# Performance work log

Measured on AMD Instinct MI355X. Metric: run time of the kernel, lower is better.

The kernel has to match this reference:

```python
import jax, jax.numpy as jnp
import numpy as np

D_MODEL = 1024
NUM_HEADS = 16
HEAD_DIM = D_MODEL // NUM_HEADS
THETA = 10000.0


def _rope(x, cos, sin):
    # x: [B, H, S, hd]; cos/sin: [S, hd//2] (broadcast over B, H)
    x_even = x[..., 0::2]
    x_odd = x[..., 1::2]
    y_even = x_even * cos - x_odd * sin
    y_odd = x_even * sin + x_odd * cos
    # interleave back: stack on last dim then flatten
    y = jnp.stack((y_even, y_odd), axis=-1)
    return y.reshape(x.shape)


def setup_inputs() -> dict:
    key = jax.random.key(0)
    ks = jax.random.split(key, 5)
    B, S = 2, 2048
    x = jax.random.normal(ks[0], (B, S, D_MODEL), dtype=jnp.float32)
    scale = 1.0 / np.sqrt(D_MODEL)
    Wq = jax.random.normal(ks[1], (D_MODEL, D_MODEL), dtype=jnp.float32) * scale
    Wk = jax.random.normal(ks[2], (D_MODEL, D_MODEL), dtype=jnp.float32) * scale
    Wv = jax.random.normal(ks[3], (D_MODEL, D_MODEL), dtype=jnp.float32) * scale
    Wo = jax.random.normal(ks[4], (D_MODEL, D_MODEL), dtype=jnp.float32) * scale
    token_positions = jnp.arange(S, dtype=jnp.int64 if jax.config.jax_enable_x64 else jnp.int32)
    return {"x": x, "token_positions": token_positions, "Wq": Wq, "Wk": Wk, "Wv": Wv, "Wo": Wo}


def reference(x, token_positions, Wq, Wk, Wv, Wo):
    B, S, _ = x.shape
    # nn.Linear(d,d,bias=False): y = x @ W.T
    q = (x @ Wq.T).reshape(B, S, NUM_HEADS, HEAD_DIM).transpose(0, 2, 1, 3)
    k = (x @ Wk.T).reshape(B, S, NUM_HEADS, HEAD_DIM).transpose(0, 2, 1, 3)
    v = (x @ Wv.T).reshape(B, S, NUM_HEADS, HEAD_DIM).transpose(0, 2, 1, 3)

    # RoPE tables gathered at token_positions
    freqs = 1.0 / THETA ** (jnp.arange(0, HEAD_DIM, 2, dtype=jnp.float32) / HEAD_DIM)
    angles = token_positions.astype(jnp.float32)[:, None] * freqs[None, :]  # [S, hd//2]
    cos, sin = jnp.cos(angles), jnp.sin(angles)
    q = _rope(q, cos, sin)
    k = _rope(k, cos, sin)

    scores = jnp.einsum("bhqd,bhkd->bhqk", q, k) / np.sqrt(HEAD_DIM)
    causal = jnp.tril(jnp.ones((S, S), dtype=bool))
    scores = jnp.where(causal, scores, jnp.finfo(scores.dtype).min)
    attn = jax.nn.softmax(scores, axis=-1)
    out = jnp.einsum("bhqk,bhkd->bhqd", attn, v)  # [B,H,S,hd]
    out = out.transpose(0, 2, 1, 3).reshape(B, S, D_MODEL)
    return out @ Wo.T
```

## Files before the change

### kernel.cpp

```cpp
#include <hip/hip_runtime.h>

#define S_LEN 2048
#define NH 16
#define HD 64
#define DM 1024
#define MTOT 4096

#define QSCALE 0.18033688011112042f

typedef short bf16x8 __attribute__((ext_vector_type(8)));
typedef float f32x4 __attribute__((ext_vector_type(4)));
typedef unsigned short u16x8 __attribute__((ext_vector_type(8)));

__device__ __forceinline__ unsigned short f2bf(float f) {
  unsigned int u = __builtin_bit_cast(unsigned int, f);
  u += 0x7fffu + ((u >> 16) & 1u);
  return (unsigned short)(u >> 16);
}
__device__ __forceinline__ unsigned short f2bf_fast(float f) {
  unsigned int u = __builtin_bit_cast(unsigned int, f);
  return (unsigned short)((u + 0x8000u) >> 16);
}

__device__ __forceinline__ void async_copy16(const void* g, void* l) {
  __builtin_amdgcn_global_load_lds(
      (const __attribute__((address_space(1))) unsigned int*)g,
      (__attribute__((address_space(3))) unsigned int*)l, 16, 0, 0);
}

__global__ void cvt_bf16_kernel(const float* __restrict__ src,
                                unsigned short* __restrict__ dst, int n) {
  int i = (blockIdx.x * 256 + threadIdx.x) * 8;
  if (i >= n) return;
  const float4* s = (const float4*)(src + i);
  float4 v0 = s[0], v1 = s[1];
  u16x8 o;
  o[0] = f2bf(v0.x); o[1] = f2bf(v0.y); o[2] = f2bf(v0.z); o[3] = f2bf(v0.w);
  o[4] = f2bf(v1.x); o[5] = f2bf(v1.y); o[6] = f2bf(v1.z); o[7] = f2bf(v1.w);
  *(u16x8*)(dst + i) = o;
}

__global__ void cvt_w_kernel(const float* __restrict__ w0, const float* __restrict__ w1,
                             const float* __restrict__ w2, const float* __restrict__ w3,
                             unsigned short* __restrict__ dst) {
  int z = blockIdx.y;
  const float* src = (z == 0) ? w0 : (z == 1) ? w1 : (z == 2) ? w2 : w3;
  int i = (blockIdx.x * 256 + threadIdx.x) * 8;
  const float4* s = (const float4*)(src + i);
  float4 v0 = s[0], v1 = s[1];
  u16x8 o;
  o[0] = f2bf(v0.x); o[1] = f2bf(v0.y); o[2] = f2bf(v0.z); o[3] = f2bf(v0.w);
  o[4] = f2bf(v1.x); o[5] = f2bf(v1.y); o[6] = f2bf(v1.z); o[7] = f2bf(v1.w);
  *(u16x8*)(dst + (size_t)z * DM * DM + i) = o;
}

__global__ void sincos_tab_kernel(const int* __restrict__ pos, float2* __restrict__ tab) {
  int idx = blockIdx.x * 256 + threadIdx.x;
  int s = idx >> 5, i = idx & 31;
  float fr = expf(-(float)i * 0.28782313662425574f);
  float ang = (float)pos[s] * fr;
  float sn, cs;
  sincosf(ang, &sn, &cs);
  tab[idx] = make_float2(cs, sn);
}

__device__ __forceinline__ void gemm_core(const unsigned short* __restrict__ A,
                                          const unsigned short* __restrict__ Bt,
                                          int m0, int n0, int K,
                                          char* a_lds, char* b_lds,
                                          f32x4 (&acc)[4][4]) {
  const int tid = threadIdx.x;
  const int w = tid >> 6, l = tid & 63;
  const int wr = w >> 1, wc = w & 1;
  const int c = l & 15, g = l >> 4;

  const size_t rs = (size_t)K * 2;
  const int lr = l >> 3;
  const int jsw = ((l & 7) ^ lr) << 4;
  const char* srcA = (const char*)A + ((size_t)m0 + w * 8 + lr) * rs + jsw;
  const char* srcB = (const char*)Bt + ((size_t)n0 + w * 8 + lr) * rs + jsw;
  char* dstA = a_lds + w * 1024 + l * 16;
  char* dstB = b_lds + w * 1024 + l * 16;
  const int csw = (c & 7) << 4;
  const int nsteps = K / 64;

  auto stage = [&](int buf, int kt) {
    const int off = buf * 16384;
#pragma unroll
    for (int i = 0; i < 4; ++i) {
      async_copy16(srcA + (size_t)i * 32 * rs + kt * 128, dstA + off + i * 4096);
      async_copy16(srcB + (size_t)i * 32 * rs + kt * 128, dstB + off + i * 4096);
    }
  };

  stage(0, 0);
  asm volatile("s_waitcnt vmcnt(0)" ::: "memory");
  __syncthreads();
  int cur = 0;

  for (int kt = 0; kt < nsteps; ++kt) {
    if (kt + 1 < nsteps) stage(cur ^ 1, kt + 1);
    const char* al = a_lds + cur * 16384;
    const char* bl = b_lds + cur * 16384;
    __builtin_amdgcn_s_setprio(1);
#pragma unroll
    for (int kk = 0; kk < 2; ++kk) {
      bf16x8 af[4], bfv[4];
#pragma unroll
      for (int mi = 0; mi < 4; ++mi)
        af[mi] = *(const bf16x8*)(al + (wr * 64 + mi * 16 + c) * 128 + ((kk * 64 + g * 16) ^ csw));
#pragma unroll
      for (int ni = 0; ni < 4; ++ni)
        bfv[ni] = *(const bf16x8*)(bl + (wc * 64 + ni * 16 + c) * 128 + ((kk * 64 + g * 16) ^ csw));
#pragma unroll
      for (int mi = 0; mi < 4; ++mi)
#pragma unroll
        for (int ni = 0; ni < 4; ++ni)
          acc[mi][ni] = __builtin_amdgcn_mfma_f32_16x16x32_bf16(af[mi], bfv[ni], acc[mi][ni], 0, 0, 0);
    }
    __builtin_amdgcn_s_setprio(0);
    asm volatile("s_waitcnt vmcnt(0)" ::: "memory");
    __syncthreads();
    cur ^= 1;
  }
}

__global__ __launch_bounds__(256)
void gemm_qkv_kernel(const unsigned short* __restrict__ X,
                     const unsigned short* __restrict__ Wq,
                     const unsigned short* __restrict__ Wk,
                     const unsigned short* __restrict__ Wv,
                     const float2* __restrict__ tab,
                     unsigned short* __restrict__ Qb,
                     unsigned short* __restrict__ Kb,
                     unsigned short* __restrict__ Vt) {
  __shared__ char a_lds[2 * 16384];
  __shared__ char b_lds[2 * 16384];
  const int z = blockIdx.z;
  const unsigned short* Bt = (z == 0) ? Wq : (z == 1) ? Wk : Wv;
  const int m0 = blockIdx.x * 128, n0 = blockIdx.y * 128;

  f32x4 acc[4][4] = {};
  gemm_core(X, Bt, m0, n0, DM, a_lds, b_lds, acc);

  const int tid = threadIdx.x;
  const int w = tid >> 6, l = tid & 63;
  const int wr = w >> 1, wc = w & 1;
  const int c = l & 15, g = l >> 4;

  if (z == 2) {
#pragma unroll
    for (int mi = 0; mi < 4; ++mi)
#pragma unroll
      for (int ni = 0; ni < 4; ++ni)
#pragma unroll
        for (int r = 0; r < 4; ++r) {
          int row = m0 + wr * 64 + mi * 16 + 4 * g + r;
          int col = n0 + wc * 64 + ni * 16 + c;
          int b = row >> 11, s = row & 2047;
          int h = col >> 6, d = col & 63;
          Vt[((size_t)(b * NH + h) * HD + d) * S_LEN + s] = f2bf(acc[mi][ni][r]);
        }
  } else {
    unsigned short* QK = z ? Kb : Qb;
    const float oscale = z ? 1.0f : QSCALE;
#pragma unroll
    for (int mi = 0; mi < 4; ++mi)
#pragma unroll
      for (int ni = 0; ni < 4; ++ni) {
        int col = n0 + wc * 64 + ni * 16 + c;
        int fi = (col >> 1) & 31;
        float sgn = (col & 1) ? 1.0f : -1.0f;
#pragma unroll
        for (int r = 0; r < 4; ++r) {
          int row = m0 + wr * 64 + mi * 16 + 4 * g + r;
          int b = row >> 11, s = row & 2047;
          float v = acc[mi][ni][r];
          float p = __shfl_xor(v, 1);
          float2 csn = tab[(s << 5) | fi];
          float vr = (v * csn.x + sgn * p * csn.y) * oscale;
          int h = col >> 6, d = col & 63;
          QK[((size_t)(b * NH + h) * S_LEN + s) * HD + d] = f2bf(vr);
        }
      }
  }
}

__global__ __launch_bounds__(256)
void gemm_out_kernel(const unsigned short* __restrict__ A,
                     const unsigned short* __restrict__ Wo,
                     float* __restrict__ out) {
  __shared__ char a_lds[2 * 16384];
  __shared__ char b_lds[2 * 16384];
  const int m0 = blockIdx.x * 128, n0 = blockIdx.y * 128;
  f32x4 acc[4][4] = {};
  gemm_core(A, Wo, m0, n0, DM, a_lds, b_lds, acc);

  const int tid = threadIdx.x;
  const int w = tid >> 6, l = tid & 63;
  const int wr = w >> 1, wc = w & 1;
  const int c = l & 15, g = l >> 4;
#pragma unroll
  for (int mi = 0; mi < 4; ++mi)
#pragma unroll
    for (int ni = 0; ni < 4; ++ni)
#pragma unroll
      for (int r = 0; r < 4; ++r) {
        int row = m0 + wr * 64 + mi * 16 + 4 * g + r;
        int col = n0 + wc * 64 + ni * 16 + c;
        out[(size_t)row * DM + col] = acc[mi][ni][r];
      }
}

__global__ __launch_bounds__(256, 4)
void attn_kernel(const unsigned short* __restrict__ Q,
                 const unsigned short* __restrict__ Kb,
                 const unsigned short* __restrict__ Vt,
                 unsigned short* __restrict__ Ob) {
  __shared__ char kbuf[2][8192];
  __shared__ char vbuf[2][8192];
  __shared__ unsigned short p_lds[4][16 * 64];
  const int tid = threadIdx.x;
  const int w = tid >> 6, l = tid & 63;
  const int g = l >> 4, c = l & 15;

  const unsigned int id = blockIdx.x;
  const int bh = id & 31;
  const int j = id >> 5;
  const int a = j & 7, kk = j >> 3;
  const int qblk = (kk == 0) ? a : (kk == 1) ? (15 - a) : (kk == 2) ? (16 + a) : (31 - a);
  const int q0 = qblk * 64;

  const size_t base = (size_t)bh * (S_LEN * HD);
  const char* Kc = (const char*)(Kb + base);
  const char* Vc = (const char*)(Vt + base);

  const int lr = l >> 3;
  const int jsw = ((l & 7) << 4) ^ (lr << 4);
  const int r0 = w * 8 + lr;
  const int r1 = (4 + w) * 8 + lr;
  const char* ksrc0 = Kc + r0 * 128 + jsw;
  const char* ksrc1 = Kc + r1 * 128 + jsw;
  const char* vsrc0 = Vc + r0 * 4096 + jsw;
  const char* vsrc1 = Vc + r1 * 4096 + jsw;

  bf16x8 qf0, qf1;
  {
    const unsigned short* qp = Q + base + (size_t)(q0 + w * 16 + c) * HD + g * 8;
    qf0 = *(const bf16x8*)qp;
    qf1 = *(const bf16x8*)(qp + 32);
  }
  f32x4 oacc[4] = {};
  float rsum[4] = {0.f, 0.f, 0.f, 0.f};
  unsigned short* pl = &p_lds[w][0];
  const int csw = (c & 7) << 4;

  auto stage = [&](int buf, int t) {
    char* kd = &kbuf[buf][w * 1024 + l * 16];
    char* vd = &vbuf[buf][w * 1024 + l * 16];
    size_t ko = (size_t)t * 8192;
    size_t vo = (size_t)t * 128;
    async_copy16(ksrc0 + ko, kd);
    async_copy16(ksrc1 + ko, kd + 4096);
    async_copy16(vsrc0 + vo, vd);
    async_copy16(vsrc1 + vo, vd + 4096);
  };

  stage(0, 0);
  asm volatile("s_waitcnt vmcnt(0)" ::: "memory");
  __syncthreads();
  int cur = 0;

  for (int t = 0; t <= qblk; ++t) {
    if (t + 1 <= qblk) stage(cur ^ 1, t + 1);
    const char* kl = kbuf[cur];
    const char* vl = vbuf[cur];
    const int kv0 = t * 64;

    f32x4 sc[4] = {};
    __builtin_amdgcn_s_setprio(1);
#pragma unroll
    for (int nt = 0; nt < 4; ++nt) {
      bf16x8 k0 = *(const bf16x8*)(kl + (nt * 16 + c) * 128 + ((g * 16) ^ csw));
      bf16x8 k1 = *(const bf16x8*)(kl + (nt * 16 + c) * 128 + ((64 + g * 16) ^ csw));
      sc[nt] = __builtin_amdgcn_mfma_f32_16x16x32_bf16(qf0, k0, sc[nt], 0, 0, 0);
      sc[nt] = __builtin_amdgcn_mfma_f32_16x16x32_bf16(qf1, k1, sc[nt], 0, 0, 0);
    }
    __builtin_amdgcn_s_setprio(0);

    if (t == qblk) {
#pragma unroll
      for (int nt = 0; nt < 4; ++nt)
#pragma unroll
        for (int r = 0; r < 4; ++r) {
          int kvi = kv0 + nt * 16 + c;
          int qi = q0 + w * 16 + 4 * g + r;
          sc[nt][r] = exp2f((kvi > qi) ? -1e30f : sc[nt][r]);
        }
    } else {
#pragma unroll
      for (int nt = 0; nt < 4; ++nt)
#pragma unroll
        for (int r = 0; r < 4; ++r)
          sc[nt][r] = exp2f(sc[nt][r]);
    }
#pragma unroll
    for (int nt = 0; nt < 4; ++nt)
#pragma unroll
      for (int r = 0; r < 4; ++r) {
        float pv = sc[nt][r];
        rsum[r] += pv;
        int row = 4 * g + r, col = nt * 16 + c;
        int byte = row * 128 + ((col * 2) ^ ((row & 7) << 4));
        *(unsigned short*)((char*)pl + byte) = f2bf_fast(pv);
      }
    asm volatile("" ::: "memory");
    __builtin_amdgcn_s_setprio(1);
#pragma unroll
    for (int ks = 0; ks < 2; ++ks) {
      int pbyte = c * 128 + ((ks * 64 + g * 16) ^ csw);
      bf16x8 pf = *(const bf16x8*)((char*)pl + pbyte);
#pragma unroll
      for (int nt = 0; nt < 4; ++nt) {
        bf16x8 vf = *(const bf16x8*)(vl + (nt * 16 + c) * 128 + ((ks * 64 + g * 16) ^ csw));
        oacc[nt] = __builtin_amdgcn_mfma_f32_16x16x32_bf16(pf, vf, oacc[nt], 0, 0, 0);
      }
    }
    __builtin_amdgcn_s_setprio(0);
    asm volatile("" ::: "memory");

    asm volatile("s_waitcnt vmcnt(0)" ::: "memory");
    __syncthreads();
    cur ^= 1;
  }

#pragma unroll
  for (int r = 0; r < 4; ++r) {
    float s = rsum[r];
    s += __shfl_xor(s, 1);
    s += __shfl_xor(s, 2);
    s += __shfl_xor(s, 4);
    s += __shfl_xor(s, 8);
    rsum[r] = 1.0f / s;
  }
  const int b = bh >> 4, h = bh & 15;
#pragma unroll
  for (int nt = 0; nt < 4; ++nt)
#pragma unroll
    for (int r = 0; r < 4; ++r) {
      int qi = q0 + w * 16 + 4 * g + r;
      int col = nt * 16 + c;
      Ob[((size_t)b * S_LEN + qi) * DM + h * HD + col] = f2bf(oacc[nt][r] * rsum[r]);
    }
}

extern "C" void kernel_launch(void* const* d_in, const int* in_sizes, int n_in,
                              void* d_out, int out_size, void* d_ws, size_t ws_size,
                              hipStream_t stream) {
  const float* x = (const float*)d_in[0];
  const int* tpos = (const int*)d_in[1];
  const float* wq = (const float*)d_in[2];
  const float* wk = (const float*)d_in[3];
  const float* wv = (const float*)d_in[4];
  const float* wo = (const float*)d_in[5];
  float* out = (float*)d_out;

  char* ws = (char*)d_ws;
  unsigned short* xb = (unsigned short*)(ws);
  unsigned short* wqb = (unsigned short*)(ws + 8388608);
  unsigned short* wkb = wqb + DM * DM;
  unsigned short* wvb = wqb + 2 * DM * DM;
  unsigned short* wob = wqb + 3 * DM * DM;
  unsigned short* qb = (unsigned short*)(ws + 16777216);
  unsigned short* kb = (unsigned short*)(ws + 16777216 + 8388608);
  unsigned short* vt = (unsigned short*)(ws + 16777216 + 2 * 8388608);
  unsigned short* ab = (unsigned short*)(ws + 16777216 + 3 * 8388608);
  float2* tab = (float2*)(ws + 50331648);

  cvt_bf16_kernel<<<2048, 256, 0, stream>>>(x, xb, MTOT * DM);
  cvt_w_kernel<<<dim3(512, 4), 256, 0, stream>>>(wq, wk, wv, wo, wqb);
  sincos_tab_kernel<<<256, 256, 0, stream>>>(tpos, tab);

  gemm_qkv_kernel<<<dim3(32, 8, 3), 256, 0, stream>>>(xb, wqb, wkb, wvb, tab, qb, kb, vt);
  attn_kernel<<<1024, 256, 0, stream>>>(qb, kb, vt, ab);
  gemm_out_kernel<<<dim3(32, 8), 256, 0, stream>>>(ab, wob, out);
}
```

Before: 126.4 us.

## Keep attention probabilities in registers via transposed MFMA and lane shuffles

Swaps the MFMA operand order so the score tile comes out transposed, with each lane holding one query row's values across kv positions. The P matrix is then packed to bf16 with v_cvt_pk_bf16_f32 and redistributed with cross-lane shuffles instead of being written to and re-read from a per-wave LDS buffer. The transposed layout also simplifies the row-sum reduction and lets the output be written as packed 8-byte stores. The cost is sixteen ds_bpermute-style shuffles per tile plus selects, in place of the LDS round trip, and the P conversion now uses the hardware round-to-nearest instruction.

```diff
diff --git a/kernel.cpp b/kernel.cpp
--- a/kernel.cpp
+++ b/kernel.cpp
@@ -11,15 +11,18 @@
 typedef short bf16x8 __attribute__((ext_vector_type(8)));
 typedef float f32x4 __attribute__((ext_vector_type(4)));
 typedef unsigned short u16x8 __attribute__((ext_vector_type(8)));
+typedef int i32x4 __attribute__((ext_vector_type(4)));
 
 __device__ __forceinline__ unsigned short f2bf(float f) {
   unsigned int u = __builtin_bit_cast(unsigned int, f);
   u += 0x7fffu + ((u >> 16) & 1u);
   return (unsigned short)(u >> 16);
 }
-__device__ __forceinline__ unsigned short f2bf_fast(float f) {
-  unsigned int u = __builtin_bit_cast(unsigned int, f);
-  return (unsigned short)((u + 0x8000u) >> 16);
+
+__device__ __forceinline__ unsigned int cvt_pk_bf16(float lo, float hi) {
+  unsigned int r;
+  asm("v_cvt_pk_bf16_f32 %0, %1, %2" : "=v"(r) : "v"(lo), "v"(hi));
+  return r;
 }
 
 __device__ __forceinline__ void async_copy16(const void* g, void* l) {
@@ -219,7 +222,6 @@
                  unsigned short* __restrict__ Ob) {
   __shared__ char kbuf[2][8192];
   __shared__ char vbuf[2][8192];
-  __shared__ unsigned short p_lds[4][16 * 64];
   const int tid = threadIdx.x;
   const int w = tid >> 6, l = tid & 63;
   const int g = l >> 4, c = l & 15;
@@ -251,9 +253,11 @@
     qf1 = *(const bf16x8*)(qp + 32);
   }
   f32x4 oacc[4] = {};
-  float rsum[4] = {0.f, 0.f, 0.f, 0.f};
-  unsigned short* pl = &p_lds[w][0];
+  float rsum = 0.f;
   const int csw = (c & 7) << 4;
+  const int srcA = (l & 15) | ((l & 16) << 1);
+  const int srcB = srcA + 16;
+  const bool hi = (l >= 32);
 
   auto stage = [&](int buf, int t) {
     char* kd = &kbuf[buf][w * 1024 + l * 16];
@@ -283,18 +287,18 @@
     for (int nt = 0; nt < 4; ++nt) {
       bf16x8 k0 = *(const bf16x8*)(kl + (nt * 16 + c) * 128 + ((g * 16) ^ csw));
       bf16x8 k1 = *(const bf16x8*)(kl + (nt * 16 + c) * 128 + ((64 + g * 16) ^ csw));
-      sc[nt] = __builtin_amdgcn_mfma_f32_16x16x32_bf16(qf0, k0, sc[nt], 0, 0, 0);
-      sc[nt] = __builtin_amdgcn_mfma_f32_16x16x32_bf16(qf1, k1, sc[nt], 0, 0, 0);
+      sc[nt] = __builtin_amdgcn_mfma_f32_16x16x32_bf16(k0, qf0, sc[nt], 0, 0, 0);
+      sc[nt] = __builtin_amdgcn_mfma_f32_16x16x32_bf16(k1, qf1, sc[nt], 0, 0, 0);
     }
     __builtin_amdgcn_s_setprio(0);
 
     if (t == qblk) {
+      const int qi = q0 + w * 16 + c;
 #pragma unroll
       for (int nt = 0; nt < 4; ++nt)
 #pragma unroll
         for (int r = 0; r < 4; ++r) {
-          int kvi = kv0 + nt * 16 + c;
-          int qi = q0 + w * 16 + 4 * g + r;
+          int kvi = kv0 + nt * 16 + 4 * g + r;
           sc[nt][r] = exp2f((kvi > qi) ? -1e30f : sc[nt][r]);
         }
     } else {
@@ -304,54 +308,59 @@
         for (int r = 0; r < 4; ++r)
           sc[nt][r] = exp2f(sc[nt][r]);
     }
-#pragma unroll
-    for (int nt = 0; nt < 4; ++nt)
-#pragma unroll
-      for (int r = 0; r < 4; ++r) {
-        float pv = sc[nt][r];
-        rsum[r] += pv;
-        int row = 4 * g + r, col = nt * 16 + c;
-        int byte = row * 128 + ((col * 2) ^ ((row & 7) << 4));
-        *(unsigned short*)((char*)pl + byte) = f2bf_fast(pv);
-      }
-    asm volatile("" ::: "memory");
+    unsigned int pk[4][2];
+#pragma unroll
+    for (int nt = 0; nt < 4; ++nt) {
+      rsum += (sc[nt][0] + sc[nt][1]) + (sc[nt][2] + sc[nt][3]);
+      pk[nt][0] = cvt_pk_bf16(sc[nt][0], sc[nt][1]);
+      pk[nt][1] = cvt_pk_bf16(sc[nt][2], sc[nt][3]);
+    }
+
     __builtin_amdgcn_s_setprio(1);
 #pragma unroll
     for (int ks = 0; ks < 2; ++ks) {
-      int pbyte = c * 128 + ((ks * 64 + g * 16) ^ csw);
-      bf16x8 pf = *(const bf16x8*)((char*)pl + pbyte);
+      int a0 = __shfl((int)pk[2 * ks][0], srcA);
+      int a1 = __shfl((int)pk[2 * ks][1], srcA);
+      int a2 = __shfl((int)pk[2 * ks][0], srcB);
+      int a3 = __shfl((int)pk[2 * ks][1], srcB);
+      int b0 = __shfl((int)pk[2 * ks + 1][0], srcA);
+      int b1 = __shfl((int)pk[2 * ks + 1][1], srcA);
+      int b2 = __shfl((int)pk[2 * ks + 1][0], srcB);
+      int b3 = __shfl((int)pk[2 * ks + 1][1], srcB);
+      i32x4 pw;
+      pw[0] = hi ? b0 : a0;
+      pw[1] = hi ? b1 : a1;
+      pw[2] = hi ? b2 : a2;
+      pw[3] = hi ? b3 : a3;
+      bf16x8 pf = __builtin_bit_cast(bf16x8, pw);
 #pragma unroll
       for (int nt = 0; nt < 4; ++nt) {
         bf16x8 vf = *(const bf16x8*)(vl + (nt * 16 + c) * 128 + ((ks * 64 + g * 16) ^ csw));
-        oacc[nt] = __builtin_amdgcn_mfma_f32_16x16x32_bf16(pf, vf, oacc[nt], 0, 0, 0);
+        oacc[nt] = __builtin_amdgcn_mfma_f32_16x16x32_bf16(vf, pf, oacc[nt], 0, 0, 0);
       }
     }
     __builtin_amdgcn_s_setprio(0);
-    asm volatile("" ::: "memory");
 
     asm volatile("s_waitcnt vmcnt(0)" ::: "memory");
     __syncthreads();
     cur ^= 1;
   }
 
-#pragma unroll
-  for (int r = 0; r < 4; ++r) {
-    float s = rsum[r];
-    s += __shfl_xor(s, 1);
-    s += __shfl_xor(s, 2);
-    s += __shfl_xor(s, 4);
-    s += __shfl_xor(s, 8);
-    rsum[r] = 1.0f / s;
-  }
+  rsum += __shfl_xor(rsum, 16);
+  rsum += __shfl_xor(rsum, 32);
+  const float inv = 1.0f / rsum;
+
   const int b = bh >> 4, h = bh & 15;
-#pragma unroll
-  for (int nt = 0; nt < 4; ++nt)
-#pragma unroll
-    for (int r = 0; r < 4; ++r) {
-      int qi = q0 + w * 16 + 4 * g + r;
-      int col = nt * 16 + c;
-      Ob[((size_t)b * S_LEN + qi) * DM + h * HD + col] = f2bf(oacc[nt][r] * rsum[r]);
-    }
+  unsigned short* dst = Ob + ((size_t)b * S_LEN + q0 + w * 16 + c) * DM + h * HD + 4 * g;
+#pragma unroll
+  for (int nt = 0; nt < 4; ++nt) {
+    unsigned int w0 = (unsigned int)f2bf(oacc[nt][0] * inv) | ((unsigned int)f2bf(oacc[nt][1] * inv) << 16);
+    unsigned int w1 = (unsigned int)f2bf(oacc[nt][2] * inv) | ((unsigned int)f2bf(oacc[nt][3] * inv) << 16);
+    uint2 pr;
+    pr.x = w0;
+    pr.y = w1;
+    *(uint2*)(dst + nt * 16) = pr;
+  }
 }
 
 extern "C" void kernel_launch(void* const* d_in, const int* in_sizes, int n_in,
```

After: 127.8 us. No clear change (+1.1%).
